# Performance work log

Measured on AMD Instinct MI355X. Metric: run time of the kernel, lower is better.

## Reference

```python
import jax, jax.numpy as jnp
import numpy as np

B, CIN, CCTX, K, V, T, KS = 8, 512, 512, 64, 256, 1024, 23
EPS = 1e-5


def _bn(z, gamma, beta):
    # train-mode BatchNorm1d over (batch, time) per channel, biased variance
    mean = jnp.mean(z, axis=(0, 2), keepdims=True)
    var = jnp.mean((z - mean) ** 2, axis=(0, 2), keepdims=True)
    return (z - mean) * jax.lax.rsqrt(var + EPS) * gamma[None, :, None] + beta[None, :, None]


def setup_inputs() -> dict:
    key = jax.random.key(0)
    ks = jax.random.split(key, 10)
    x = jax.random.normal(ks[0], (B, CIN, T), dtype=jnp.float32)
    context = jax.random.normal(ks[1], (B, CCTX, T), dtype=jnp.float32)
    Wq = jax.random.normal(ks[2], (K, CIN), dtype=jnp.float32) * (CIN ** -0.5)
    bq = jnp.zeros((K,), dtype=jnp.float32)
    Wk = jax.random.normal(ks[3], (K, CCTX), dtype=jnp.float32) * (CCTX ** -0.5)
    bk = jnp.zeros((K,), dtype=jnp.float32)
    Wv = jax.random.normal(ks[4], (V, CCTX), dtype=jnp.float32) * (CCTX ** -0.5)
    bv = jnp.zeros((V,), dtype=jnp.float32)
    gamma_q = jnp.ones((K,), dtype=jnp.float32)
    beta_q = jnp.zeros((K,), dtype=jnp.float32)
    gamma_v = jnp.ones((V,), dtype=jnp.float32)
    beta_v = jnp.zeros((V,), dtype=jnp.float32)
    pos_w = jax.random.normal(ks[5], (K, KS), dtype=jnp.float32) * (KS ** -0.5)
    pos_b = jnp.zeros((K,), dtype=jnp.float32)
    return {"x": x, "context": context, "Wq": Wq, "bq": bq, "Wk": Wk, "bk": bk,
            "Wv": Wv, "bv": bv, "gamma_q": gamma_q, "beta_q": beta_q,
            "gamma_v": gamma_v, "beta_v": beta_v, "pos_w": pos_w, "pos_b": pos_b}


def reference(x, context, Wq, bq, Wk, bk, Wv, bv,
              gamma_q, beta_q, gamma_v, beta_v, pos_w, pos_b):
    # 1x1 conv1d == channel matmul
    queries = jnp.einsum('bct,kc->bkt', x, Wq) + bq[None, :, None]          # (B,K,T)
    keys = jnp.einsum('bct,kc->bkt', context, Wk) + bk[None, :, None]       # (B,K,T)
    values = jnp.einsum('bct,vc->bvt', context, Wv) + bv[None, :, None]     # (B,V,T)

    norm_keys = jax.nn.softmax(keys, axis=-1)                               # softmax over T
    queries = _bn(queries, gamma_q, beta_q)
    values = _bn(values, gamma_v, beta_v)

    q_t = jnp.transpose(queries, (0, 2, 1))                                 # (B,T,K)
    v_t = jnp.transpose(values, (0, 2, 1))                                  # (B,T,V)

    content_lambda = jnp.einsum('bkt,btv->bkv', norm_keys, v_t)             # (B,K,V)

    # positional conv2d: kernel (K,1,KS,1), padding (KS//2, 0) along T
    lhs = v_t[:, None, :, :]                                                # (B,1,T,V)
    rhs = pos_w[:, None, :, None]                                           # (K,1,KS,1)
    pl = jax.lax.conv_general_dilated(
        lhs, rhs, window_strides=(1, 1),
        padding=[(KS // 2, KS // 2), (0, 0)],
        dimension_numbers=('NCHW', 'OIHW', 'NCHW'))
    pl = pl + pos_b[None, :, None, None]                                    # (B,K,T,V)
    pl = jnp.transpose(pl, (0, 2, 1, 3))                                    # (B,T,K,V)

    content_out = jnp.einsum('btk,bkv->btv', q_t, content_lambda)           # (B,T,V)
    positional_out = jnp.einsum('btk,btkv->btv', q_t, pl)                   # (B,T,V)

    return jnp.transpose(content_out + positional_out, (0, 2, 1))           # (B,V,T)
```

## Files before the change

### kernel.cpp

```cpp
#include <hip/hip_runtime.h>
#include <math.h>

#define B_ 8
#define CIN_ 512
#define K_ 64
#define V_ 256
#define T_ 1024
#define KS_ 23
#define EPS_ 1e-5f
#define NTC_ 16

typedef __attribute__((ext_vector_type(8))) short bf16x8;
typedef __attribute__((ext_vector_type(4))) float f32x4;

__device__ __forceinline__ unsigned short f2bf(float f) {
    union { float f; unsigned u; } x; x.f = f;
    unsigned r = x.u + 0x7fffu + ((x.u >> 16) & 1u);
    return (unsigned short)(r >> 16);
}
__device__ __forceinline__ float bf2f(unsigned short h) {
    union { unsigned u; float f; } x; x.u = ((unsigned)h) << 16;
    return x.f;
}

__global__ __launch_bounds__(256) void cvtT_kernel(
    const float* __restrict__ x, const float* __restrict__ ctx,
    unsigned short* __restrict__ xT, unsigned short* __restrict__ cT)
{
    __shared__ unsigned short sh[64][72];
    const int tid = threadIdx.x;
    const int t0 = blockIdx.x * 64, c0 = blockIdx.y * 64;
    const int b = blockIdx.z & 7, which = blockIdx.z >> 3;
    const float* src = which ? ctx : x;
    unsigned short* dst = which ? cT : xT;

    const int cl = tid >> 2, qq = tid & 3;
    const float* row = src + ((size_t)b * CIN_ + c0 + cl) * T_ + t0 + qq * 16;
    #pragma unroll
    for (int u = 0; u < 4; u++) {
        float4 f = *(const float4*)(row + 4 * u);
        sh[qq * 16 + 4 * u + 0][cl] = f2bf(f.x);
        sh[qq * 16 + 4 * u + 1][cl] = f2bf(f.y);
        sh[qq * 16 + 4 * u + 2][cl] = f2bf(f.z);
        sh[qq * 16 + 4 * u + 3][cl] = f2bf(f.w);
    }
    __syncthreads();
    const int tl = tid >> 2;
    unsigned short* orow = dst + ((size_t)b * T_ + t0 + tl) * CIN_ + c0 + qq * 16;
    *(bf16x8*)(orow)     = *(bf16x8*)&sh[tl][qq * 16];
    *(bf16x8*)(orow + 8) = *(bf16x8*)&sh[tl][qq * 16 + 8];
}

__global__ __launch_bounds__(256) void prew_kernel(
    const float* __restrict__ Wq, const float* __restrict__ Wk,
    const float* __restrict__ Wv, unsigned short* __restrict__ Wb,
    float* __restrict__ stat)
{
    if (blockIdx.x == 0 && threadIdx.x < 160)
        ((float4*)stat)[threadIdx.x] = make_float4(0.f, 0.f, 0.f, 0.f);
    const int i4 = blockIdx.x * 256 + threadIdx.x;
    const int n1 = K_ * CIN_ / 4, n2 = 2 * K_ * CIN_ / 4;
    const float* src; int off;
    if (i4 < n1)      { src = Wq; off = i4; }
    else if (i4 < n2) { src = Wk; off = i4 - n1; }
    else              { src = Wv; off = i4 - n2; }
    float4 f = ((const float4*)src)[off];
    ushort4 h;
    h.x = f2bf(f.x); h.y = f2bf(f.y); h.z = f2bf(f.z); h.w = f2bf(f.w);
    *(ushort4*)(Wb + (size_t)i4 * 4) = h;
}

__global__ __launch_bounds__(256) void proj_mfma3(
    const unsigned short* __restrict__ xT, const unsigned short* __restrict__ cT,
    const unsigned short* __restrict__ Wb,
    const float* __restrict__ bq, const float* __restrict__ bk,
    const float* __restrict__ bv,
    float* __restrict__ k_buf, float* __restrict__ v_raw,
    unsigned short* __restrict__ qT, float* __restrict__ stat)
{
    __shared__ unsigned short Wt[64][72];
    __shared__ unsigned short Xt[128][72];
    const int tid = threadIdx.x;
    const int b = blockIdx.z, t0 = blockIdx.x * 128, yb = blockIdx.y;

    const unsigned short* in; const unsigned short* W; const float* bias;
    float* outp = nullptr; int ch0 = 0; float* ssum = nullptr; float* ssq = nullptr;
    if (yb == 0)      { in = xT; W = Wb;             bias = bq;
                        ssum = stat; ssq = stat + 64; ch0 = 0; }
    else if (yb == 1) { in = cT; W = Wb + K_ * CIN_; bias = bk;
                        outp = k_buf + (size_t)b * K_ * T_; }
    else { int m0 = (yb - 2) * 64; in = cT;
           W = Wb + 2 * K_ * CIN_ + (size_t)m0 * CIN_; bias = bv + m0;
           outp = v_raw + ((size_t)b * V_ + m0) * T_;
           ssum = stat + 128; ssq = stat + 384; ch0 = m0; }

    const int lane = tid & 63, w = tid >> 6;
    const int col = lane & 15, quad = lane >> 4;
    const int wm = tid >> 2, wp = tid & 3;
    const int xt = tid >> 1, xh = tid & 1;

    f32x4 acc[8];
    #pragma unroll
    for (int j = 0; j < 8; j++) acc[j] = (f32x4){0.f, 0.f, 0.f, 0.f};

    for (int c0 = 0; c0 < CIN_; c0 += 64) {
        {
            const unsigned short* ws = W + (size_t)wm * CIN_ + c0 + wp * 16;
            *(bf16x8*)&Wt[wm][wp * 16]     = *(const bf16x8*)(ws);
            *(bf16x8*)&Wt[wm][wp * 16 + 8] = *(const bf16x8*)(ws + 8);
            const unsigned short* xs = in + ((size_t)b * T_ + t0 + xt) * CIN_ + c0 + xh * 32;
            #pragma unroll
            for (int u = 0; u < 4; u++)
                *(bf16x8*)&Xt[xt][xh * 32 + 8 * u] = *(const bf16x8*)(xs + 8 * u);
        }
        __syncthreads();
        #pragma unroll
        for (int ks = 0; ks < 2; ks++) {
            const int kc = ks * 32 + quad * 8;
            bf16x8 af = *(bf16x8*)&Wt[w * 16 + col][kc];
            #pragma unroll
            for (int j = 0; j < 8; j++) {
                bf16x8 bfr = *(bf16x8*)&Xt[j * 16 + col][kc];
                acc[j] = __builtin_amdgcn_mfma_f32_16x16x32_bf16(af, bfr, acc[j], 0, 0, 0);
            }
        }
        __syncthreads();
    }

    float bias_v[4], s[4], sq[4];
    #pragma unroll
    for (int r = 0; r < 4; r++) {
        bias_v[r] = bias[w * 16 + quad * 4 + r];
        s[r] = 0.f; sq[r] = 0.f;
    }
    #pragma unroll
    for (int j = 0; j < 8; j++) {
        float o[4];
        #pragma unroll
        for (int r = 0; r < 4; r++) {
            o[r] = acc[j][r] + bias_v[r];
            s[r] += o[r]; sq[r] += o[r] * o[r];
        }
        if (yb == 0) {
            ushort4 h;
            h.x = f2bf(o[0]); h.y = f2bf(o[1]); h.z = f2bf(o[2]); h.w = f2bf(o[3]);
            *(ushort4*)(qT + ((size_t)b * T_ + t0 + j * 16 + col) * K_ + w * 16 + quad * 4) = h;
        } else {
            #pragma unroll
            for (int r = 0; r < 4; r++)
                outp[(size_t)(w * 16 + quad * 4 + r) * T_ + t0 + j * 16 + col] = o[r];
        }
    }
    if (ssum) {
        #pragma unroll
        for (int r = 0; r < 4; r++) {
            float sv = s[r], qv = sq[r];
            #pragma unroll
            for (int off = 1; off < 16; off <<= 1) {
                sv += __shfl_xor(sv, off, 64);
                qv += __shfl_xor(qv, off, 64);
            }
            if (col == 0) {
                int ch = ch0 + w * 16 + quad * 4 + r;
                atomicAdd(&ssum[ch], sv);
                atomicAdd(&ssq[ch], qv);
            }
        }
    }
}

__global__ __launch_bounds__(256) void softmax_kernel(float* __restrict__ k_buf)
{
    __shared__ float red[256];
    const int tid = threadIdx.x;
    float4* row = (float4*)(k_buf + (size_t)blockIdx.x * T_);
    float4 v = row[tid];
    float mx = fmaxf(fmaxf(v.x, v.y), fmaxf(v.z, v.w));
    red[tid] = mx; __syncthreads();
    for (int st = 128; st > 0; st >>= 1) {
        if (tid < st) red[tid] = fmaxf(red[tid], red[tid + st]);
        __syncthreads();
    }
    mx = red[0]; __syncthreads();
    float4 e;
    e.x = __expf(v.x - mx); e.y = __expf(v.y - mx);
    e.z = __expf(v.z - mx); e.w = __expf(v.w - mx);
    red[tid] = e.x + e.y + e.z + e.w; __syncthreads();
    for (int st = 128; st > 0; st >>= 1) {
        if (tid < st) red[tid] += red[tid + st];
        __syncthreads();
    }
    float inv = 1.f / red[0];
    e.x *= inv; e.y *= inv; e.z *= inv; e.w *= inv;
    row[tid] = e;
}

__global__ __launch_bounds__(256) void lambda_kernel3(
    const float* __restrict__ k_buf, const float* __restrict__ v_raw,
    float* __restrict__ clp)
{
    __shared__ __align__(16) float nks[K_][68];
    __shared__ __align__(16) float vls[64][68];
    const int tid = threadIdx.x;
    const int b = blockIdx.z, v0 = blockIdx.y * 64, tc = blockIdx.x, t0 = tc * 64;
    {
        const int r = tid >> 2, q = tid & 3;
        const float* nrow = k_buf + ((size_t)b * K_ + r) * T_ + t0;
        const float* vrow = v_raw + ((size_t)b * V_ + v0 + r) * T_ + t0;
        #pragma unroll
        for (int i = 0; i < 4; i++) {
            int c4 = q + 4 * i;
            float4 g = *(const float4*)(nrow + 4 * c4);
            *(float4*)&nks[r][4 * c4] = g;
            float4 h = *(const float4*)(vrow + 4 * c4);
            vls[4 * c4 + 0][r] = h.x; vls[4 * c4 + 1][r] = h.y;
            vls[4 * c4 + 2][r] = h.z; vls[4 * c4 + 3][r] = h.w;
        }
    }
    __syncthreads();
    const int tv = tid & 15, tk = tid >> 4;
    float4 acc[4];
    #pragma unroll
    for (int i = 0; i < 4; i++) acc[i] = make_float4(0.f, 0.f, 0.f, 0.f);
    for (int tt = 0; tt < 16; tt++) {
        float4 w0 = *(float4*)&vls[4 * tt + 0][4 * tv];
        float4 w1 = *(float4*)&vls[4 * tt + 1][4 * tv];
        float4 w2 = *(float4*)&vls[4 * tt + 2][4 * tv];
        float4 w3 = *(float4*)&vls[4 * tt + 3][4 * tv];
        #pragma unroll
        for (int i = 0; i < 4; i++) {
            float4 n = *(float4*)&nks[4 * tk + i][4 * tt];
            acc[i] += w0 * n.x + w1 * n.y + w2 * n.z + w3 * n.w;
        }
    }
    #pragma unroll
    for (int i = 0; i < 4; i++)
        *(float4*)&clp[(((size_t)b * NTC_ + tc) * K_ + 4 * tk + i) * V_ + v0 + 4 * tv] = acc[i];
}

__global__ __launch_bounds__(256) void prep_cl_kernel2(
    const float* __restrict__ clp, const float* __restrict__ stat,
    const float* __restrict__ gq, const float* __restrict__ betaq,
    const float* __restrict__ gv, const float* __restrict__ betav,
    unsigned short* __restrict__ clb2, float* __restrict__ hterm)
{
    __shared__ float qsc[64], qsh[64], red[4][64];
    const int tid = threadIdx.x;
    const int b = blockIdx.y, v0 = blockIdx.x * 64;
    const float inv_n = 1.f / (B_ * T_);
    if (tid < 64) {
        float mean = stat[tid] * inv_n;
        float var  = stat[64 + tid] * inv_n - mean * mean;
        float sc = gq[tid] * rsqrtf(var + EPS_);
        qsc[tid] = sc; qsh[tid] = betaq[tid] - mean * sc;
    }
    const int vl = tid & 63, kq = tid >> 6;
    const int c = v0 + vl;
    float vmean = stat[128 + c] * inv_n;
    float vvar  = stat[384 + c] * inv_n - vmean * vmean;
    float vsv = gv[c] * rsqrtf(vvar + EPS_);
    float vhv = betav[c] - vmean * vsv;
    __syncthreads();
    float h = 0.f;
    for (int kk = 0; kk < 16; kk++) {
        int k = kq * 16 + kk;
        float a = 0.f;
        #pragma unroll
        for (int tc = 0; tc < NTC_; tc++)
            a += clp[(((size_t)b * NTC_ + tc) * K_ + k) * V_ + c];
        float clbv = a * vsv + vhv;
        h += qsh[k] * clbv;
        clb2[((size_t)b * V_ + c) * K_ + k] = f2bf(clbv * qsc[k]);
    }
    red[kq][vl] = h;
    __syncthreads();
    if (tid < 64)
        hterm[(size_t)b * V_ + v0 + tid] =
            red[0][tid] + red[1][tid] + red[2][tid] + red[3][tid];
}

__global__ __launch_bounds__(256) void out_kernel4(
    const unsigned short* __restrict__ qT, const unsigned short* __restrict__ clb2,
    const float* __restrict__ hterm, const float* __restrict__ v_raw,
    const float* __restrict__ stat,
    const float* __restrict__ gq, const float* __restrict__ betaq,
    const float* __restrict__ gv, const float* __restrict__ betav,
    const float* __restrict__ pos_w, const float* __restrict__ pos_b,
    float* __restrict__ out)
{
    __shared__ unsigned short qTt[64][72];
    __shared__ unsigned short clv[64][72];
    __shared__ float vs2T[88][68];
    __shared__ float qpt[64][24];
    __shared__ float pws[64][24];
    __shared__ float qsc[64], qsh[64];
    __shared__ float consts[24];
    __shared__ float hvs[64];
    const int tid = threadIdx.x;
    const int b = blockIdx.z, v0 = blockIdx.y * 64, t0 = blockIdx.x * 64;
    const float inv_n = 1.f / (B_ * T_);

    if (tid < 64) {
        float mean = stat[tid] * inv_n;
        float var  = stat[64 + tid] * inv_n - mean * mean;
        float sc = gq[tid] * rsqrtf(var + EPS_);
        qsc[tid] = sc; qsh[tid] = betaq[tid] - mean * sc;
        hvs[tid] = hterm[(size_t)b * V_ + v0 + tid];
    }
    {
        const int rl = tid >> 2, part = tid & 3;
        const unsigned short* qs = qT + ((size_t)b * T_ + t0 + rl) * K_ + part * 16;
        *(bf16x8*)&qTt[rl][part * 16]     = *(const bf16x8*)(qs);
        *(bf16x8*)&qTt[rl][part * 16 + 8] = *(const bf16x8*)(qs + 8);
        const unsigned short* cs = clb2 + ((size_t)b * V_ + v0 + rl) * K_ + part * 16;
        *(bf16x8*)&clv[rl][part * 16]     = *(const bf16x8*)(cs);
        *(bf16x8*)&clv[rl][part * 16 + 8] = *(const bf16x8*)(cs + 8);
    }
    {
        const int vl = tid >> 2, qq = tid & 3;
        const int c = v0 + vl;
        float vmean = stat[128 + c] * inv_n;
        float vvar  = stat[384 + c] * inv_n - vmean * vmean;
        float vsv = gv[c] * rsqrtf(vvar + EPS_);
        float vhv = betav[c] - vmean * vsv;
        const float* vrow = v_raw + ((size_t)b * V_ + c) * T_;
        #pragma unroll
        for (int i = 0; i < 22; i++) {
            int cc = qq + 4 * i;
            if (cc < 86) {
                int t = t0 + cc - 11;
                vs2T[cc][vl] = (t >= 0 && t < T_) ? vrow[t] * vsv + vhv : 0.f;
            }
        }
    }
    __syncthreads();

    for (int idx = tid; idx < K_ * 24; idx += 256) {
        int k = idx / 24, s = idx % 24;
        pws[k][s] = qsc[k] * (s < KS_ ? pos_w[k * KS_ + s] : pos_b[k]);
    }
    if (tid < 24) {
        float cs = 0.f;
        for (int k = 0; k < K_; k++)
            cs += qsh[k] * (tid < KS_ ? pos_w[k * KS_ + tid] : pos_b[k]);
        consts[tid] = cs;
    }
    __syncthreads();

    {
        const int t = tid >> 2, sg = tid & 3, s0 = sg * 6;
        float a[6];
        #pragma unroll
        for (int u = 0; u < 6; u++) a[u] = consts[s0 + u];
        #pragma unroll
        for (int kb = 0; kb < 8; kb++) {
            bf16x8 qv = *(bf16x8*)&qTt[t][kb * 8];
            #pragma unroll
            for (int j = 0; j < 8; j++) {
                float q = bf2f((unsigned short)qv[j]);
                #pragma unroll
                for (int u = 0; u < 6; u++) a[u] += q * pws[kb * 8 + j][s0 + u];
            }
        }
        #pragma unroll
        for (int u = 0; u < 6; u++) qpt[t][s0 + u] = a[u];
    }
    __syncthreads();

    const int lane = tid & 63, w = tid >> 6;
    const int col = lane & 15, quad = lane >> 4;

    f32x4 acc[4];
    #pragma unroll
    for (int tf = 0; tf < 4; tf++) acc[tf] = (f32x4){0.f, 0.f, 0.f, 0.f};

    #pragma unroll
    for (int ks = 0; ks < 2; ks++) {
        const int kc = ks * 32 + quad * 8;
        bf16x8 af = *(bf16x8*)&clv[w * 16 + col][kc];
        #pragma unroll
        for (int tf = 0; tf < 4; tf++) {
            bf16x8 bq = *(bf16x8*)&qTt[tf * 16 + col][kc];
            acc[tf] = __builtin_amdgcn_mfma_f32_16x16x32_bf16(af, bq, acc[tf], 0, 0, 0);
        }
    }

    const int vb = w * 16 + quad * 4;
    float4 hv4 = *(float4*)&hvs[vb];
    #pragma unroll
    for (int tf = 0; tf < 4; tf++) {
        const int lt = tf * 16 + col;
        float qv[24];
        #pragma unroll
        for (int u = 0; u < 6; u++)
            *(float4*)&qv[4 * u] = *(float4*)&qpt[lt][4 * u];
        float4 a; a.x = acc[tf][0]; a.y = acc[tf][1]; a.z = acc[tf][2]; a.w = acc[tf][3];
        #pragma unroll
        for (int s = 0; s < KS_; s++) {
            float4 wv = *(float4*)&vs2T[lt + s][vb];
            a.x += qv[s] * wv.x; a.y += qv[s] * wv.y;
            a.z += qv[s] * wv.z; a.w += qv[s] * wv.w;
        }
        float base = qv[23];
        a.x += base + hv4.x; a.y += base + hv4.y;
        a.z += base + hv4.z; a.w += base + hv4.w;
        float* ap = (float*)&a;
        #pragma unroll
        for (int r = 0; r < 4; r++)
            out[((size_t)b * V_ + v0 + vb + r) * T_ + t0 + lt] = ap[r];
    }
}

extern "C" void kernel_launch(void* const* d_in, const int* in_sizes, int n_in,
                              void* d_out, int out_size, void* d_ws, size_t ws_size,
                              hipStream_t stream)
{
    const float* x     = (const float*)d_in[0];
    const float* ctx   = (const float*)d_in[1];
    const float* Wq    = (const float*)d_in[2];
    const float* bq    = (const float*)d_in[3];
    const float* Wk    = (const float*)d_in[4];
    const float* bk    = (const float*)d_in[5];
    const float* Wv    = (const float*)d_in[6];
    const float* bv    = (const float*)d_in[7];
    const float* gq    = (const float*)d_in[8];
    const float* betaq = (const float*)d_in[9];
    const float* gv    = (const float*)d_in[10];
    const float* betav = (const float*)d_in[11];
    const float* pos_w = (const float*)d_in[12];
    const float* pos_b = (const float*)d_in[13];
    float* out = (float*)d_out;

    float* ws    = (float*)d_ws;
    float* k_buf = ws;
    float* v_raw = k_buf + (size_t)B_ * K_ * T_;
    float* clp   = v_raw + (size_t)B_ * V_ * T_;
    float* stat  = clp + (size_t)B_ * NTC_ * K_ * V_;
    float* hterm = stat + 640;
    unsigned short* xT   = (unsigned short*)(hterm + (size_t)B_ * V_);
    unsigned short* cT   = xT + (size_t)B_ * T_ * CIN_;
    unsigned short* Wb   = cT + (size_t)B_ * T_ * CIN_;
    unsigned short* qT   = Wb + (size_t)(2 * K_ + V_) * CIN_;
    unsigned short* clb2 = qT + (size_t)B_ * T_ * K_;

    cvtT_kernel<<<dim3(T_ / 64, CIN_ / 64, 2 * B_), 256, 0, stream>>>(x, ctx, xT, cT);
    prew_kernel<<<dim3((2 * K_ + V_) * CIN_ / 1024), 256, 0, stream>>>(Wq, Wk, Wv, Wb, stat);
    proj_mfma3<<<dim3(T_ / 128, 6, B_), 256, 0, stream>>>(
        xT, cT, Wb, bq, bk, bv, k_buf, v_raw, qT, stat);
    softmax_kernel<<<dim3(B_ * K_), 256, 0, stream>>>(k_buf);
    lambda_kernel3<<<dim3(NTC_, V_ / 64, B_), 256, 0, stream>>>(k_buf, v_raw, clp);
    prep_cl_kernel2<<<dim3(V_ / 64, B_), 256, 0, stream>>>(
        clp, stat, gq, betaq, gv, betav, clb2, hterm);
    out_kernel4<<<dim3(T_ / 64, V_ / 64, B_), 256, 0, stream>>>(
        qT, clb2, hterm, v_raw, stat, gq, betaq, gv, betav, pos_w, pos_b, out);
}
```

Before: 161.4 us.

## Fuse softmax, lambda reduction and BN prep into one kernel; merge prep launches

The key softmax, the content-lambda contraction and the BatchNorm/lambda prep step now run in a single kernel. It computes an online max and sum per key row, applies the softmax on the fly while loading tiles, and loops over all T chunks inside each block. This removes the partial-sum buffer and two kernel launches. The input transpose and weight conversion kernels are also merged into one launch. In exchange the fused stage runs on only 32 blocks, each streaming the full time axis serially, and the softmax statistics are recomputed redundantly by each V-block.

Result: slower. 223.0 us (+38.1%).

```diff
diff --git a/kernel.cpp b/kernel.cpp
--- a/kernel.cpp
+++ b/kernel.cpp
@@ -8,7 +8,6 @@
 #define T_ 1024
 #define KS_ 23
 #define EPS_ 1e-5f
-#define NTC_ 16
 
 typedef __attribute__((ext_vector_type(8))) short bf16x8;
 typedef __attribute__((ext_vector_type(4))) float f32x4;
@@ -23,51 +22,51 @@
     return x.f;
 }
 
-__global__ __launch_bounds__(256) void cvtT_kernel(
+__global__ __launch_bounds__(256) void prep_kernel(
     const float* __restrict__ x, const float* __restrict__ ctx,
-    unsigned short* __restrict__ xT, unsigned short* __restrict__ cT)
+    const float* __restrict__ Wq, const float* __restrict__ Wk,
+    const float* __restrict__ Wv,
+    unsigned short* __restrict__ xT, unsigned short* __restrict__ cT,
+    unsigned short* __restrict__ Wb, float* __restrict__ stat)
 {
     __shared__ unsigned short sh[64][72];
     const int tid = threadIdx.x;
-    const int t0 = blockIdx.x * 64, c0 = blockIdx.y * 64;
-    const int b = blockIdx.z & 7, which = blockIdx.z >> 3;
-    const float* src = which ? ctx : x;
-    unsigned short* dst = which ? cT : xT;
-
-    const int cl = tid >> 2, qq = tid & 3;
-    const float* row = src + ((size_t)b * CIN_ + c0 + cl) * T_ + t0 + qq * 16;
-    #pragma unroll
-    for (int u = 0; u < 4; u++) {
-        float4 f = *(const float4*)(row + 4 * u);
-        sh[qq * 16 + 4 * u + 0][cl] = f2bf(f.x);
-        sh[qq * 16 + 4 * u + 1][cl] = f2bf(f.y);
-        sh[qq * 16 + 4 * u + 2][cl] = f2bf(f.z);
-        sh[qq * 16 + 4 * u + 3][cl] = f2bf(f.w);
-    }
-    __syncthreads();
-    const int tl = tid >> 2;
-    unsigned short* orow = dst + ((size_t)b * T_ + t0 + tl) * CIN_ + c0 + qq * 16;
-    *(bf16x8*)(orow)     = *(bf16x8*)&sh[tl][qq * 16];
-    *(bf16x8*)(orow + 8) = *(bf16x8*)&sh[tl][qq * 16 + 8];
-}
-
-__global__ __launch_bounds__(256) void prew_kernel(
-    const float* __restrict__ Wq, const float* __restrict__ Wk,
-    const float* __restrict__ Wv, unsigned short* __restrict__ Wb,
-    float* __restrict__ stat)
-{
-    if (blockIdx.x == 0 && threadIdx.x < 160)
-        ((float4*)stat)[threadIdx.x] = make_float4(0.f, 0.f, 0.f, 0.f);
-    const int i4 = blockIdx.x * 256 + threadIdx.x;
-    const int n1 = K_ * CIN_ / 4, n2 = 2 * K_ * CIN_ / 4;
-    const float* src; int off;
-    if (i4 < n1)      { src = Wq; off = i4; }
-    else if (i4 < n2) { src = Wk; off = i4 - n1; }
-    else              { src = Wv; off = i4 - n2; }
-    float4 f = ((const float4*)src)[off];
-    ushort4 h;
-    h.x = f2bf(f.x); h.y = f2bf(f.y); h.z = f2bf(f.z); h.w = f2bf(f.w);
-    *(ushort4*)(Wb + (size_t)i4 * 4) = h;
+    const int id = blockIdx.x;
+    if (id < 2048) {
+        const int t0 = (id & 15) * 64, c0 = ((id >> 4) & 7) * 64;
+        const int z = id >> 7, b = z & 7, which = z >> 3;
+        const float* src = which ? ctx : x;
+        unsigned short* dst = which ? cT : xT;
+        const int cl = tid >> 2, qq = tid & 3;
+        const float* row = src + ((size_t)b * CIN_ + c0 + cl) * T_ + t0 + qq * 16;
+        #pragma unroll
+        for (int u = 0; u < 4; u++) {
+            float4 f = *(const float4*)(row + 4 * u);
+            sh[qq * 16 + 4 * u + 0][cl] = f2bf(f.x);
+            sh[qq * 16 + 4 * u + 1][cl] = f2bf(f.y);
+            sh[qq * 16 + 4 * u + 2][cl] = f2bf(f.z);
+            sh[qq * 16 + 4 * u + 3][cl] = f2bf(f.w);
+        }
+        __syncthreads();
+        const int tl = tid >> 2;
+        unsigned short* orow = dst + ((size_t)b * T_ + t0 + tl) * CIN_ + c0 + qq * 16;
+        *(bf16x8*)(orow)     = *(bf16x8*)&sh[tl][qq * 16];
+        *(bf16x8*)(orow + 8) = *(bf16x8*)&sh[tl][qq * 16 + 8];
+    } else {
+        const int wid = id - 2048;
+        if (wid == 0 && tid < 160)
+            ((float4*)stat)[tid] = make_float4(0.f, 0.f, 0.f, 0.f);
+        const int i4 = wid * 256 + tid;
+        const int n1 = K_ * CIN_ / 4, n2 = 2 * K_ * CIN_ / 4;
+        const float* src; int off;
+        if (i4 < n1)      { src = Wq; off = i4; }
+        else if (i4 < n2) { src = Wk; off = i4 - n1; }
+        else              { src = Wv; off = i4 - n2; }
+        float4 f = ((const float4*)src)[off];
+        ushort4 h;
+        h.x = f2bf(f.x); h.y = f2bf(f.y); h.z = f2bf(f.z); h.w = f2bf(f.w);
+        *(ushort4*)(Wb + (size_t)i4 * 4) = h;
+    }
 }
 
 __global__ __launch_bounds__(256) void proj_mfma3(
@@ -169,114 +168,126 @@
     }
 }
 
-__global__ __launch_bounds__(256) void softmax_kernel(float* __restrict__ k_buf)
-{
-    __shared__ float red[256];
-    const int tid = threadIdx.x;
-    float4* row = (float4*)(k_buf + (size_t)blockIdx.x * T_);
-    float4 v = row[tid];
-    float mx = fmaxf(fmaxf(v.x, v.y), fmaxf(v.z, v.w));
-    red[tid] = mx; __syncthreads();
-    for (int st = 128; st > 0; st >>= 1) {
-        if (tid < st) red[tid] = fmaxf(red[tid], red[tid + st]);
-        __syncthreads();
-    }
-    mx = red[0]; __syncthreads();
-    float4 e;
-    e.x = __expf(v.x - mx); e.y = __expf(v.y - mx);
-    e.z = __expf(v.z - mx); e.w = __expf(v.w - mx);
-    red[tid] = e.x + e.y + e.z + e.w; __syncthreads();
-    for (int st = 128; st > 0; st >>= 1) {
-        if (tid < st) red[tid] += red[tid + st];
-        __syncthreads();
-    }
-    float inv = 1.f / red[0];
-    e.x *= inv; e.y *= inv; e.z *= inv; e.w *= inv;
-    row[tid] = e;
-}
-
-__global__ __launch_bounds__(256) void lambda_kernel3(
+__global__ __launch_bounds__(256) void slc_kernel(
     const float* __restrict__ k_buf, const float* __restrict__ v_raw,
-    float* __restrict__ clp)
-{
-    __shared__ __align__(16) float nks[K_][68];
-    __shared__ __align__(16) float vls[64][68];
-    const int tid = threadIdx.x;
-    const int b = blockIdx.z, v0 = blockIdx.y * 64, tc = blockIdx.x, t0 = tc * 64;
-    {
-        const int r = tid >> 2, q = tid & 3;
-        const float* nrow = k_buf + ((size_t)b * K_ + r) * T_ + t0;
-        const float* vrow = v_raw + ((size_t)b * V_ + v0 + r) * T_ + t0;
-        #pragma unroll
-        for (int i = 0; i < 4; i++) {
-            int c4 = q + 4 * i;
-            float4 g = *(const float4*)(nrow + 4 * c4);
-            *(float4*)&nks[r][4 * c4] = g;
-            float4 h = *(const float4*)(vrow + 4 * c4);
-            vls[4 * c4 + 0][r] = h.x; vls[4 * c4 + 1][r] = h.y;
-            vls[4 * c4 + 2][r] = h.z; vls[4 * c4 + 3][r] = h.w;
-        }
-    }
-    __syncthreads();
-    const int tv = tid & 15, tk = tid >> 4;
-    float4 acc[4];
-    #pragma unroll
-    for (int i = 0; i < 4; i++) acc[i] = make_float4(0.f, 0.f, 0.f, 0.f);
-    for (int tt = 0; tt < 16; tt++) {
-        float4 w0 = *(float4*)&vls[4 * tt + 0][4 * tv];
-        float4 w1 = *(float4*)&vls[4 * tt + 1][4 * tv];
-        float4 w2 = *(float4*)&vls[4 * tt + 2][4 * tv];
-        float4 w3 = *(float4*)&vls[4 * tt + 3][4 * tv];
-        #pragma unroll
-        for (int i = 0; i < 4; i++) {
-            float4 n = *(float4*)&nks[4 * tk + i][4 * tt];
-            acc[i] += w0 * n.x + w1 * n.y + w2 * n.z + w3 * n.w;
-        }
-    }
-    #pragma unroll
-    for (int i = 0; i < 4; i++)
-        *(float4*)&clp[(((size_t)b * NTC_ + tc) * K_ + 4 * tk + i) * V_ + v0 + 4 * tv] = acc[i];
-}
-
-__global__ __launch_bounds__(256) void prep_cl_kernel2(
-    const float* __restrict__ clp, const float* __restrict__ stat,
+    const float* __restrict__ stat,
     const float* __restrict__ gq, const float* __restrict__ betaq,
     const float* __restrict__ gv, const float* __restrict__ betav,
     unsigned short* __restrict__ clb2, float* __restrict__ hterm)
 {
-    __shared__ float qsc[64], qsh[64], red[4][64];
+    __shared__ __align__(16) float nks[K_][68];
+    __shared__ __align__(16) float vls[64][68];
+    __shared__ float mrow[64], lrow[64];
+    __shared__ float ml4[64][4][2];
+    __shared__ float qsc[64], qsh[64];
+    __shared__ float redh[16][68];
     const int tid = threadIdx.x;
     const int b = blockIdx.y, v0 = blockIdx.x * 64;
     const float inv_n = 1.f / (B_ * T_);
+
     if (tid < 64) {
         float mean = stat[tid] * inv_n;
         float var  = stat[64 + tid] * inv_n - mean * mean;
         float sc = gq[tid] * rsqrtf(var + EPS_);
         qsc[tid] = sc; qsh[tid] = betaq[tid] - mean * sc;
     }
-    const int vl = tid & 63, kq = tid >> 6;
-    const int c = v0 + vl;
-    float vmean = stat[128 + c] * inv_n;
-    float vvar  = stat[384 + c] * inv_n - vmean * vmean;
-    float vsv = gv[c] * rsqrtf(vvar + EPS_);
-    float vhv = betav[c] - vmean * vsv;
-    __syncthreads();
-    float h = 0.f;
-    for (int kk = 0; kk < 16; kk++) {
-        int k = kq * 16 + kk;
-        float a = 0.f;
-        #pragma unroll
-        for (int tc = 0; tc < NTC_; tc++)
-            a += clp[(((size_t)b * NTC_ + tc) * K_ + k) * V_ + c];
-        float clbv = a * vsv + vhv;
-        h += qsh[k] * clbv;
-        clb2[((size_t)b * V_ + c) * K_ + k] = f2bf(clbv * qsc[k]);
-    }
-    red[kq][vl] = h;
-    __syncthreads();
-    if (tid < 64)
-        hterm[(size_t)b * V_ + v0 + tid] =
-            red[0][tid] + red[1][tid] + red[2][tid] + red[3][tid];
+
+    {
+        const int r = tid >> 2, j = tid & 3;
+        const float4* krow = (const float4*)(k_buf + ((size_t)b * K_ + r) * T_);
+        float m = -1e30f, l = 0.f;
+        for (int i = 0; i < 64; i++) {
+            float4 v = krow[j + 4 * i];
+            float mx = fmaxf(fmaxf(v.x, v.y), fmaxf(v.z, v.w));
+            float mn = fmaxf(m, mx);
+            l = l * __expf(m - mn) + __expf(v.x - mn) + __expf(v.y - mn)
+              + __expf(v.z - mn) + __expf(v.w - mn);
+            m = mn;
+        }
+        ml4[r][j][0] = m; ml4[r][j][1] = l;
+    }
+    __syncthreads();
+    if (tid < 64) {
+        float mm = -1e30f;
+        #pragma unroll
+        for (int u = 0; u < 4; u++) mm = fmaxf(mm, ml4[tid][u][0]);
+        float ll = 0.f;
+        #pragma unroll
+        for (int u = 0; u < 4; u++) ll += ml4[tid][u][1] * __expf(ml4[tid][u][0] - mm);
+        mrow[tid] = mm; lrow[tid] = 1.f / ll;
+    }
+    __syncthreads();
+
+    const int tv = tid & 15, tk = tid >> 4;
+    float4 acc[4];
+    #pragma unroll
+    for (int i = 0; i < 4; i++) acc[i] = make_float4(0.f, 0.f, 0.f, 0.f);
+
+    for (int tc = 0; tc < 16; tc++) {
+        const int t0 = tc * 64;
+        {
+            const int rr = tid >> 2, q = tid & 3;
+            const float* nrow = k_buf + ((size_t)b * K_ + rr) * T_ + t0;
+            const float* vrow = v_raw + ((size_t)b * V_ + v0 + rr) * T_ + t0;
+            const float mr = mrow[rr], li = lrow[rr];
+            #pragma unroll
+            for (int i = 0; i < 4; i++) {
+                int c4 = q + 4 * i;
+                float4 g = *(const float4*)(nrow + 4 * c4);
+                g.x = __expf(g.x - mr) * li; g.y = __expf(g.y - mr) * li;
+                g.z = __expf(g.z - mr) * li; g.w = __expf(g.w - mr) * li;
+                *(float4*)&nks[rr][4 * c4] = g;
+                float4 h = *(const float4*)(vrow + 4 * c4);
+                vls[4 * c4 + 0][rr] = h.x; vls[4 * c4 + 1][rr] = h.y;
+                vls[4 * c4 + 2][rr] = h.z; vls[4 * c4 + 3][rr] = h.w;
+            }
+        }
+        __syncthreads();
+        for (int tt = 0; tt < 16; tt++) {
+            float4 w0 = *(float4*)&vls[4 * tt + 0][4 * tv];
+            float4 w1 = *(float4*)&vls[4 * tt + 1][4 * tv];
+            float4 w2 = *(float4*)&vls[4 * tt + 2][4 * tv];
+            float4 w3 = *(float4*)&vls[4 * tt + 3][4 * tv];
+            #pragma unroll
+            for (int i = 0; i < 4; i++) {
+                float4 n = *(float4*)&nks[4 * tk + i][4 * tt];
+                acc[i] += w0 * n.x + w1 * n.y + w2 * n.z + w3 * n.w;
+            }
+        }
+        __syncthreads();
+    }
+
+    const int cb = v0 + 4 * tv;
+    float vsv[4], vhv[4];
+    #pragma unroll
+    for (int jj = 0; jj < 4; jj++) {
+        int c = cb + jj;
+        float mean = stat[128 + c] * inv_n;
+        float var  = stat[384 + c] * inv_n - mean * mean;
+        vsv[jj] = gv[c] * rsqrtf(var + EPS_);
+        vhv[jj] = betav[c] - mean * vsv[jj];
+    }
+    float hpart[4] = {0.f, 0.f, 0.f, 0.f};
+    #pragma unroll
+    for (int i = 0; i < 4; i++) {
+        int k = 4 * tk + i;
+        float* ap = (float*)&acc[i];
+        #pragma unroll
+        for (int jj = 0; jj < 4; jj++) {
+            float clbv = ap[jj] * vsv[jj] + vhv[jj];
+            hpart[jj] += qsh[k] * clbv;
+            clb2[((size_t)b * V_ + cb + jj) * K_ + k] = f2bf(clbv * qsc[k]);
+        }
+    }
+    #pragma unroll
+    for (int jj = 0; jj < 4; jj++) redh[tk][4 * tv + jj] = hpart[jj];
+    __syncthreads();
+    if (tid < 64) {
+        float h = 0.f;
+        #pragma unroll
+        for (int u = 0; u < 16; u++) h += redh[u][tid];
+        hterm[(size_t)b * V_ + v0 + tid] = h;
+    }
 }
 
 __global__ __launch_bounds__(256) void out_kernel4(
@@ -434,8 +445,7 @@
     float* ws    = (float*)d_ws;
     float* k_buf = ws;
     float* v_raw = k_buf + (size_t)B_ * K_ * T_;
-    float* clp   = v_raw + (size_t)B_ * V_ * T_;
-    float* stat  = clp + (size_t)B_ * NTC_ * K_ * V_;
+    float* stat  = v_raw + (size_t)B_ * V_ * T_;
     float* hterm = stat + 640;
     unsigned short* xT   = (unsigned short*)(hterm + (size_t)B_ * V_);
     unsigned short* cT   = xT + (size_t)B_ * T_ * CIN_;
@@ -443,14 +453,12 @@
     unsigned short* qT   = Wb + (size_t)(2 * K_ + V_) * CIN_;
     unsigned short* clb2 = qT + (size_t)B_ * T_ * K_;
 
-    cvtT_kernel<<<dim3(T_ / 64, CIN_ / 64, 2 * B_), 256, 0, stream>>>(x, ctx, xT, cT);
-    prew_kernel<<<dim3((2 * K_ + V_) * CIN_ / 1024), 256, 0, stream>>>(Wq, Wk, Wv, Wb, stat);
+    prep_kernel<<<dim3(2048 + 192), 256, 0, stream>>>(
+        x, ctx, Wq, Wk, Wv, xT, cT, Wb, stat);
     proj_mfma3<<<dim3(T_ / 128, 6, B_), 256, 0, stream>>>(
         xT, cT, Wb, bq, bk, bv, k_buf, v_raw, qT, stat);
-    softmax_kernel<<<dim3(B_ * K_), 256, 0, stream>>>(k_buf);
-    lambda_kernel3<<<dim3(NTC_, V_ / 64, B_), 256, 0, stream>>>(k_buf, v_raw, clp);
-    prep_cl_kernel2<<<dim3(V_ / 64, B_), 256, 0, stream>>>(
-        clp, stat, gq, betaq, gv, betav, clb2, hterm);
+    slc_kernel<<<dim3(V_ / 64, B_), 256, 0, stream>>>(
+        k_buf, v_raw, stat, gq, betaq, gv, betav, clb2, hterm);
     out_kernel4<<<dim3(T_ / 64, V_ / 64, B_), 256, 0, stream>>>(
         qT, clb2, hterm, v_raw, stat, gq, betaq, gv, betav, pos_w, pos_b, out);
 }
```
